# Optimization experiments

Hardware: AMD Instinct MI355X
Metric: run time of the kernel (lower is better)

## Reference

```python
import jax, jax.numpy as jnp
import numpy as np

B, T, I, H = 2048, 1024, 4, 16

def setup_inputs() -> dict:
    key = jax.random.key(0)
    ks = jax.random.split(key, 8)
    s_ih = 1.0 / np.sqrt(H)
    # PyTorch LSTM params: gate order [i, f, g, o], each block of size H
    W_ih = jax.random.uniform(ks[0], (4 * H, I), jnp.float32, -s_ih, s_ih)
    W_hh = jax.random.uniform(ks[1], (4 * H, H), jnp.float32, -s_ih, s_ih)
    b_ih = jax.random.uniform(ks[2], (4 * H,), jnp.float32, -s_ih, s_ih)
    b_hh = jax.random.uniform(ks[3], (4 * H,), jnp.float32, -s_ih, s_ih)
    W_d = jax.random.uniform(ks[4], (1, H), jnp.float32, -s_ih, s_ih)
    b_d = jax.random.uniform(ks[5], (1,), jnp.float32, -s_ih, s_ih)
    x = jax.random.normal(ks[6], (B, T, I), jnp.float32)
    return {"x": x, "W_ih": W_ih, "W_hh": W_hh, "b_ih": b_ih, "b_hh": b_hh, "W_d": W_d, "b_d": b_d}

def _lstm(x, W_ih, W_hh, b_ih, b_hh):
    # Precompute input projections for all timesteps: [B, T, 4H]
    xw = jnp.einsum('bti,gi->btg', x, W_ih) + b_ih + b_hh
    xw = jnp.swapaxes(xw, 0, 1)  # [T, B, 4H] for scan
    h0 = jnp.zeros((x.shape[0], W_hh.shape[1]), x.dtype)
    c0 = jnp.zeros_like(h0)
    Hh = W_hh.shape[1]

    def step(carry, xw_t):
        h, c = carry
        gates = xw_t + h @ W_hh.T  # [B, 4H]
        i = jax.nn.sigmoid(gates[:, 0*Hh:1*Hh])
        f = jax.nn.sigmoid(gates[:, 1*Hh:2*Hh])
        g = jnp.tanh(gates[:, 2*Hh:3*Hh])
        o = jax.nn.sigmoid(gates[:, 3*Hh:4*Hh])
        c = f * c + i * g
        h = o * jnp.tanh(c)
        return (h, c), h

    _, hs = jax.lax.scan(step, (h0, c0), xw)  # hs: [T, B, H]
    return jnp.swapaxes(hs, 0, 1)  # [B, T, H]

def reference(x, W_ih, W_hh, b_ih, b_hh, W_d, b_d):
    lstm_out = _lstm(x, W_ih, W_hh, b_ih, b_hh)
    return jax.nn.sigmoid(lstm_out @ W_d.T + b_d)  # [B, T, 1]
```

## Files before the change

kernel.cpp:

```cpp
#include <hip/hip_runtime.h>


#define T_DIM 1024
#define LOG2E 1.4426950408889634f

__device__ __forceinline__ float fsig(float x) {
    float e = __builtin_amdgcn_exp2f(-x * LOG2E);
    return __builtin_amdgcn_rcpf(1.0f + e);
}

template<int CTRL>
__device__ __forceinline__ float dpp_f(float v) {
    int i = __float_as_int(v);
    return __int_as_float(__builtin_amdgcn_update_dpp(i, i, CTRL, 0xF, 0xF, false));
}

__device__ __forceinline__ float swz16(float v) {
    return __int_as_float(__builtin_amdgcn_ds_swizzle(__float_as_int(v), 0x401F));
}

__global__ __launch_bounds__(64) void lstm_disc_kernel(
    const float* __restrict__ x,
    const float* __restrict__ W_ih,
    const float* __restrict__ W_hh,
    const float* __restrict__ b_ih,
    const float* __restrict__ b_hh,
    const float* __restrict__ W_d,
    const float* __restrict__ b_d,
    float* __restrict__ out)
{
    const int tid  = threadIdx.x;
    const int half = tid >> 5;
    const int s    = tid & 31;
    const int j    = s & 15;
    const int hi   = (s >> 4) & 1;
    const int batch = blockIdx.x * 2 + half;
    const int r1 = s, r2 = s + 32;

    float W1p[16], W2p[16], Wdp[16];
#pragma unroll
    for (int k = 0; k < 16; ++k) {
        const int jx = j ^ k;
        W1p[k] = W_hh[r1 * 16 + jx];
        W2p[k] = W_hh[r2 * 16 + jx];
        Wdp[k] = W_d[jx];
    }
    const float4 Wx1 = *reinterpret_cast<const float4*>(W_ih + r1 * 4);
    const float4 Wx2 = *reinterpret_cast<const float4*>(W_ih + r2 * 4);
    const float bias1 = b_ih[r1] + b_hh[r1];
    const float bias2 = b_ih[r2] + b_hh[r2];
    const float bd = b_d[0];
    const float m2  = hi ? 1.0f : 2.0f;
    const float m2c = m2 - 1.0f;

    const float4* xp = reinterpret_cast<const float4*>(x + (size_t)batch * (T_DIM * 4));
    float4 xv = xp[0];

    float h = 0.0f, c = 0.0f;
    float s0 = 0.f, s1 = 0.f, s2 = 0.f, s3 = 0.f;

    for (int t4 = 0; t4 < T_DIM; t4 += 4) {
#pragma unroll
        for (int u = 0; u < 4; ++u) {
            const int t = t4 + u;
            const float4 xn = xp[(t + 1 < T_DIM) ? (t + 1) : (T_DIM - 1)];

            float A0 = W1p[0] * h, B0 = W2p[0] * h, P0 = Wdp[0] * h;
            float A1 = 0.f, B1 = 0.f, P1 = 0.f;

            const float v1 = dpp_f<0xB1>(h);
            const float v2 = dpp_f<0x4E>(h);
            const float v3 = dpp_f<0x1B>(h);
            const float m7 = dpp_f<0x141>(h);
            const float mF = dpp_f<0x140>(h);
            A1 = fmaf(W1p[1], v1, A1); B1 = fmaf(W2p[1], v1, B1); P1 = fmaf(Wdp[1], v1, P1);
            A0 = fmaf(W1p[2], v2, A0); B0 = fmaf(W2p[2], v2, B0); P0 = fmaf(Wdp[2], v2, P0);
            A1 = fmaf(W1p[3], v3, A1); B1 = fmaf(W2p[3], v3, B1); P1 = fmaf(Wdp[3], v3, P1);
            const float v6 = dpp_f<0xB1>(m7);
            const float v5 = dpp_f<0x4E>(m7);
            const float v4 = dpp_f<0x1B>(m7);
            const float m8 = dpp_f<0x141>(mF);
            A0 = fmaf(W1p[7], m7, A0); B0 = fmaf(W2p[7], m7, B0); P0 = fmaf(Wdp[7], m7, P0);
            A1 = fmaf(W1p[6], v6, A1); B1 = fmaf(W2p[6], v6, B1); P1 = fmaf(Wdp[6], v6, P1);
            A0 = fmaf(W1p[5], v5, A0); B0 = fmaf(W2p[5], v5, B0); P0 = fmaf(Wdp[5], v5, P0);
            A1 = fmaf(W1p[4], v4, A1); B1 = fmaf(W2p[4], v4, B1); P1 = fmaf(Wdp[4], v4, P1);
            const float vE = dpp_f<0xB1>(mF);
            const float vD = dpp_f<0x4E>(mF);
            const float vC = dpp_f<0x1B>(mF);
            A0 = fmaf(W1p[15], mF, A0); B0 = fmaf(W2p[15], mF, B0); P0 = fmaf(Wdp[15], mF, P0);
            A1 = fmaf(W1p[14], vE, A1); B1 = fmaf(W2p[14], vE, B1); P1 = fmaf(Wdp[14], vE, P1);
            A0 = fmaf(W1p[13], vD, A0); B0 = fmaf(W2p[13], vD, B0); P0 = fmaf(Wdp[13], vD, P0);
            A1 = fmaf(W1p[12], vC, A1); B1 = fmaf(W2p[12], vC, B1); P1 = fmaf(Wdp[12], vC, P1);
            const float v9 = dpp_f<0xB1>(m8);
            const float vA = dpp_f<0x4E>(m8);
            const float vB = dpp_f<0x1B>(m8);
            A0 = fmaf(W1p[8],  m8, A0); B0 = fmaf(W2p[8],  m8, B0); P0 = fmaf(Wdp[8],  m8, P0);
            A1 = fmaf(W1p[9],  v9, A1); B1 = fmaf(W2p[9],  v9, B1); P1 = fmaf(Wdp[9],  v9, P1);
            A0 = fmaf(W1p[10], vA, A0); B0 = fmaf(W2p[10], vA, B0); P0 = fmaf(Wdp[10], vA, P0);
            A1 = fmaf(W1p[11], vB, A1); B1 = fmaf(W2p[11], vB, B1); P1 = fmaf(Wdp[11], vB, P1);

            float g1 = fmaf(Wx1.x, xv.x, fmaf(Wx1.y, xv.y, fmaf(Wx1.z, xv.z, fmaf(Wx1.w, xv.w, bias1))));
            float g2 = fmaf(Wx2.x, xv.x, fmaf(Wx2.y, xv.y, fmaf(Wx2.z, xv.z, fmaf(Wx2.w, xv.w, bias2))));
            g1 += A0 + A1;
            g2 += B0 + B1;

            const float oo = fsig((P0 + P1) + bd);
            if (u == 1) s0 = oo;
            else if (u == 2) s1 = oo;
            else if (u == 3) s2 = oo;
            else {
                s3 = oo;
                if (t4 > 0 && (tid & 31) == 0)
                    *reinterpret_cast<float4*>(out + (size_t)batch * T_DIM + (t4 - 4)) =
                        make_float4(s0, s1, s2, s3);
            }

            const float act1 = fsig(g1);
            const float act2 = fmaf(m2, fsig(m2 * g2), -m2c);
            const float sw1 = swz16(act1);
            const float sw2 = swz16(act2);
            const float ig = hi ? (sw1 * sw2) : (act1 * act2);
            const float f  = hi ? act1 : sw1;
            const float o  = hi ? act2 : sw2;
            c = fmaf(f, c, ig);
            const float tc = fmaf(2.0f, fsig(2.0f * c), -1.0f);
            h = o * tc;

            xv = xn;
        }
    }

    {
        float P0 = Wdp[0] * h, P1 = 0.f;
        const float v1 = dpp_f<0xB1>(h);
        const float v2 = dpp_f<0x4E>(h);
        const float v3 = dpp_f<0x1B>(h);
        const float m7 = dpp_f<0x141>(h);
        const float mF = dpp_f<0x140>(h);
        P1 = fmaf(Wdp[1], v1, P1); P0 = fmaf(Wdp[2], v2, P0); P1 = fmaf(Wdp[3], v3, P1);
        const float v6 = dpp_f<0xB1>(m7);
        const float v5 = dpp_f<0x4E>(m7);
        const float v4 = dpp_f<0x1B>(m7);
        const float m8 = dpp_f<0x141>(mF);
        P0 = fmaf(Wdp[7], m7, P0); P1 = fmaf(Wdp[6], v6, P1);
        P0 = fmaf(Wdp[5], v5, P0); P1 = fmaf(Wdp[4], v4, P1);
        const float vE = dpp_f<0xB1>(mF);
        const float vD = dpp_f<0x4E>(mF);
        const float vC = dpp_f<0x1B>(mF);
        P0 = fmaf(Wdp[15], mF, P0); P1 = fmaf(Wdp[14], vE, P1);
        P0 = fmaf(Wdp[13], vD, P0); P1 = fmaf(Wdp[12], vC, P1);
        const float v9 = dpp_f<0xB1>(m8);
        const float vA = dpp_f<0x4E>(m8);
        const float vB = dpp_f<0x1B>(m8);
        P0 = fmaf(Wdp[8],  m8, P0); P1 = fmaf(Wdp[9],  v9, P1);
        P0 = fmaf(Wdp[10], vA, P0); P1 = fmaf(Wdp[11], vB, P1);

        s3 = fsig((P0 + P1) + bd);
        if ((tid & 31) == 0)
            *reinterpret_cast<float4*>(out + (size_t)batch * T_DIM + (T_DIM - 4)) =
                make_float4(s0, s1, s2, s3);
    }
}

extern "C" void kernel_launch(void* const* d_in, const int* in_sizes, int n_in,
                              void* d_out, int out_size, void* d_ws, size_t ws_size,
                              hipStream_t stream) {
    const float* x    = (const float*)d_in[0];
    const float* W_ih = (const float*)d_in[1];
    const float* W_hh = (const float*)d_in[2];
    const float* b_ih = (const float*)d_in[3];
    const float* b_hh = (const float*)d_in[4];
    const float* W_d  = (const float*)d_in[5];
    const float* b_d  = (const float*)d_in[6];
    float* out = (float*)d_out;

    lstm_disc_kernel<<<1024, 64, 0, stream>>>(x, W_ih, W_hh, b_ih, b_hh, W_d, b_d, out);
}
```

Baseline: 339.9 us.

## Map one batch per wave with one gate row per lane

```diff
diff --git a/kernel.cpp b/kernel.cpp
--- a/kernel.cpp
+++ b/kernel.cpp
@@ -3,6 +3,8 @@
 
 #define T_DIM 1024
 #define LOG2E 1.4426950408889634f
+
+typedef __attribute__((ext_vector_type(2))) int i32x2;
 
 __device__ __forceinline__ float fsig(float x) {
     float e = __builtin_amdgcn_exp2f(-x * LOG2E);
@@ -19,6 +21,16 @@
     return __int_as_float(__builtin_amdgcn_ds_swizzle(__float_as_int(v), 0x401F));
 }
 
+__device__ __forceinline__ float xchg32(float v, bool hi32) {
+#if __has_builtin(__builtin_amdgcn_permlane32_swap)
+    i32x2 pr = __builtin_amdgcn_permlane32_swap(__float_as_int(v), __float_as_int(v), false, false);
+    return __int_as_float(hi32 ? pr[0] : pr[1]);
+#else
+    int l = threadIdx.x & 63;
+    return __int_as_float(__builtin_amdgcn_ds_bpermute(((l ^ 32) << 2), __float_as_int(v)));
+#endif
+}
+
 __global__ __launch_bounds__(64) void lstm_disc_kernel(
     const float* __restrict__ x,
     const float* __restrict__ W_ih,
@@ -29,35 +41,28 @@
     const float* __restrict__ b_d,
     float* __restrict__ out)
 {
-    const int tid  = threadIdx.x;
-    const int half = tid >> 5;
-    const int s    = tid & 31;
-    const int j    = s & 15;
-    const int hi   = (s >> 4) & 1;
-    const int batch = blockIdx.x * 2 + half;
-    const int r1 = s, r2 = s + 32;
+    const int l  = threadIdx.x;
+    const int j  = l & 15;
+    const bool s1 = (l & 16) != 0;
+    const bool s2 = (l & 32) != 0;
+    const int batch = blockIdx.x;
 
-    float W1p[16], W2p[16], Wdp[16];
+    float Wp[16];
 #pragma unroll
-    for (int k = 0; k < 16; ++k) {
-        const int jx = j ^ k;
-        W1p[k] = W_hh[r1 * 16 + jx];
-        W2p[k] = W_hh[r2 * 16 + jx];
-        Wdp[k] = W_d[jx];
-    }
-    const float4 Wx1 = *reinterpret_cast<const float4*>(W_ih + r1 * 4);
-    const float4 Wx2 = *reinterpret_cast<const float4*>(W_ih + r2 * 4);
-    const float bias1 = b_ih[r1] + b_hh[r1];
-    const float bias2 = b_ih[r2] + b_hh[r2];
+    for (int k = 0; k < 16; ++k) Wp[k] = W_hh[l * 16 + (j ^ k)];
+    const float4 Wx = *reinterpret_cast<const float4*>(W_ih + l * 4);
+    const float bias = b_ih[l] + b_hh[l];
+    const float wd = W_d[j];
     const float bd = b_d[0];
-    const float m2  = hi ? 1.0f : 2.0f;
-    const float m2c = m2 - 1.0f;
+    const bool isg = s2 && !s1;
+    const float m2  = isg ? 2.0f : 1.0f;
+    const float m2n = isg ? -1.0f : 0.0f;
 
     const float4* xp = reinterpret_cast<const float4*>(x + (size_t)batch * (T_DIM * 4));
     float4 xv = xp[0];
 
     float h = 0.0f, c = 0.0f;
-    float s0 = 0.f, s1 = 0.f, s2 = 0.f, s3 = 0.f;
+    float s0v = 0.f, s1v = 0.f, s2v = 0.f;
 
     for (int t4 = 0; t4 < T_DIM; t4 += 4) {
 #pragma unroll
@@ -65,100 +70,77 @@
             const int t = t4 + u;
             const float4 xn = xp[(t + 1 < T_DIM) ? (t + 1) : (T_DIM - 1)];
 
-            float A0 = W1p[0] * h, B0 = W2p[0] * h, P0 = Wdp[0] * h;
-            float A1 = 0.f, B1 = 0.f, P1 = 0.f;
+            const float gx = fmaf(Wx.x, xv.x, fmaf(Wx.y, xv.y,
+                               fmaf(Wx.z, xv.z, fmaf(Wx.w, xv.w, bias))));
 
+            float a0 = fmaf(Wp[0], h, gx);
             const float v1 = dpp_f<0xB1>(h);
             const float v2 = dpp_f<0x4E>(h);
             const float v3 = dpp_f<0x1B>(h);
             const float m7 = dpp_f<0x141>(h);
             const float mF = dpp_f<0x140>(h);
-            A1 = fmaf(W1p[1], v1, A1); B1 = fmaf(W2p[1], v1, B1); P1 = fmaf(Wdp[1], v1, P1);
-            A0 = fmaf(W1p[2], v2, A0); B0 = fmaf(W2p[2], v2, B0); P0 = fmaf(Wdp[2], v2, P0);
-            A1 = fmaf(W1p[3], v3, A1); B1 = fmaf(W2p[3], v3, B1); P1 = fmaf(Wdp[3], v3, P1);
+            float a1 = Wp[1] * v1;
+            float a2 = Wp[2] * v2;
+            float a3 = Wp[3] * v3;
             const float v6 = dpp_f<0xB1>(m7);
             const float v5 = dpp_f<0x4E>(m7);
             const float v4 = dpp_f<0x1B>(m7);
             const float m8 = dpp_f<0x141>(mF);
-            A0 = fmaf(W1p[7], m7, A0); B0 = fmaf(W2p[7], m7, B0); P0 = fmaf(Wdp[7], m7, P0);
-            A1 = fmaf(W1p[6], v6, A1); B1 = fmaf(W2p[6], v6, B1); P1 = fmaf(Wdp[6], v6, P1);
-            A0 = fmaf(W1p[5], v5, A0); B0 = fmaf(W2p[5], v5, B0); P0 = fmaf(Wdp[5], v5, P0);
-            A1 = fmaf(W1p[4], v4, A1); B1 = fmaf(W2p[4], v4, B1); P1 = fmaf(Wdp[4], v4, P1);
+            a0 = fmaf(Wp[7], m7, a0);
+            a1 = fmaf(Wp[6], v6, a1);
+            a2 = fmaf(Wp[5], v5, a2);
+            a3 = fmaf(Wp[4], v4, a3);
             const float vE = dpp_f<0xB1>(mF);
             const float vD = dpp_f<0x4E>(mF);
             const float vC = dpp_f<0x1B>(mF);
-            A0 = fmaf(W1p[15], mF, A0); B0 = fmaf(W2p[15], mF, B0); P0 = fmaf(Wdp[15], mF, P0);
-            A1 = fmaf(W1p[14], vE, A1); B1 = fmaf(W2p[14], vE, B1); P1 = fmaf(Wdp[14], vE, P1);
-            A0 = fmaf(W1p[13], vD, A0); B0 = fmaf(W2p[13], vD, B0); P0 = fmaf(Wdp[13], vD, P0);
-            A1 = fmaf(W1p[12], vC, A1); B1 = fmaf(W2p[12], vC, B1); P1 = fmaf(Wdp[12], vC, P1);
+            a0 = fmaf(Wp[15], mF, a0);
+            a1 = fmaf(Wp[14], vE, a1);
+            a2 = fmaf(Wp[13], vD, a2);
+            a3 = fmaf(Wp[12], vC, a3);
             const float v9 = dpp_f<0xB1>(m8);
             const float vA = dpp_f<0x4E>(m8);
             const float vB = dpp_f<0x1B>(m8);
-            A0 = fmaf(W1p[8],  m8, A0); B0 = fmaf(W2p[8],  m8, B0); P0 = fmaf(Wdp[8],  m8, P0);
-            A1 = fmaf(W1p[9],  v9, A1); B1 = fmaf(W2p[9],  v9, B1); P1 = fmaf(Wdp[9],  v9, P1);
-            A0 = fmaf(W1p[10], vA, A0); B0 = fmaf(W2p[10], vA, B0); P0 = fmaf(Wdp[10], vA, P0);
-            A1 = fmaf(W1p[11], vB, A1); B1 = fmaf(W2p[11], vB, B1); P1 = fmaf(Wdp[11], vB, P1);
+            a0 = fmaf(Wp[8],  m8, a0);
+            a1 = fmaf(Wp[9],  v9, a1);
+            a2 = fmaf(Wp[10], vA, a2);
+            a3 = fmaf(Wp[11], vB, a3);
+            const float g = (a0 + a1) + (a2 + a3);
 
-            float g1 = fmaf(Wx1.x, xv.x, fmaf(Wx1.y, xv.y, fmaf(Wx1.z, xv.z, fmaf(Wx1.w, xv.w, bias1))));
-            float g2 = fmaf(Wx2.x, xv.x, fmaf(Wx2.y, xv.y, fmaf(Wx2.z, xv.z, fmaf(Wx2.w, xv.w, bias2))));
-            g1 += A0 + A1;
-            g2 += B0 + B1;
+            const float act = fmaf(m2, fsig(m2 * g), m2n);
 
-            const float oo = fsig((P0 + P1) + bd);
-            if (u == 1) s0 = oo;
-            else if (u == 2) s1 = oo;
-            else if (u == 3) s2 = oo;
-            else {
-                s3 = oo;
-                if (t4 > 0 && (tid & 31) == 0)
-                    *reinterpret_cast<float4*>(out + (size_t)batch * T_DIM + (t4 - 4)) =
-                        make_float4(s0, s1, s2, s3);
-            }
+            const float b16 = swz16(act);
+            const float b32 = xchg32(act, s2);
+            const float b48 = swz16(b32);
+            const float pa = s1 ? b16 : act;
+            const float pb = s1 ? b48 : b32;
+            const float ig = pa * pb;
+            const float f1 = s2 ? b48 : b16;
+            const float f2 = s2 ? b32 : act;
+            const float fg = s1 ? f2 : f1;
+            const float o1 = s2 ? b16 : b48;
+            const float o2 = s2 ? act : b32;
+            const float og = s1 ? o2 : o1;
 
-            const float act1 = fsig(g1);
-            const float act2 = fmaf(m2, fsig(m2 * g2), -m2c);
-            const float sw1 = swz16(act1);
-            const float sw2 = swz16(act2);
-            const float ig = hi ? (sw1 * sw2) : (act1 * act2);
-            const float f  = hi ? act1 : sw1;
-            const float o  = hi ? act2 : sw2;
-            c = fmaf(f, c, ig);
+            c = fmaf(fg, c, ig);
             const float tc = fmaf(2.0f, fsig(2.0f * c), -1.0f);
-            h = o * tc;
+            h = og * tc;
+
+            float p = h * wd;
+            p += dpp_f<0xB1>(p);
+            p += dpp_f<0x4E>(p);
+            p += dpp_f<0x124>(p);
+            p += dpp_f<0x128>(p);
+            const float oo = fsig(p + bd);
+
+            if (u == 0) s0v = oo;
+            else if (u == 1) s1v = oo;
+            else if (u == 2) s2v = oo;
+            else if (l == 0)
+                *reinterpret_cast<float4*>(out + (size_t)batch * T_DIM + t4) =
+                    make_float4(s0v, s1v, s2v, oo);
 
             xv = xn;
         }
-    }
-
-    {
-        float P0 = Wdp[0] * h, P1 = 0.f;
-        const float v1 = dpp_f<0xB1>(h);
-        const float v2 = dpp_f<0x4E>(h);
-        const float v3 = dpp_f<0x1B>(h);
-        const float m7 = dpp_f<0x141>(h);
-        const float mF = dpp_f<0x140>(h);
-        P1 = fmaf(Wdp[1], v1, P1); P0 = fmaf(Wdp[2], v2, P0); P1 = fmaf(Wdp[3], v3, P1);
-        const float v6 = dpp_f<0xB1>(m7);
-        const float v5 = dpp_f<0x4E>(m7);
-        const float v4 = dpp_f<0x1B>(m7);
-        const float m8 = dpp_f<0x141>(mF);
-        P0 = fmaf(Wdp[7], m7, P0); P1 = fmaf(Wdp[6], v6, P1);
-        P0 = fmaf(Wdp[5], v5, P0); P1 = fmaf(Wdp[4], v4, P1);
-        const float vE = dpp_f<0xB1>(mF);
-        const float vD = dpp_f<0x4E>(mF);
-        const float vC = dpp_f<0x1B>(mF);
-        P0 = fmaf(Wdp[15], mF, P0); P1 = fmaf(Wdp[14], vE, P1);
-        P0 = fmaf(Wdp[13], vD, P0); P1 = fmaf(Wdp[12], vC, P1);
-        const float v9 = dpp_f<0xB1>(m8);
-        const float vA = dpp_f<0x4E>(m8);
-        const float vB = dpp_f<0x1B>(m8);
-        P0 = fmaf(Wdp[8],  m8, P0); P1 = fmaf(Wdp[9],  v9, P1);
-        P0 = fmaf(Wdp[10], vA, P0); P1 = fmaf(Wdp[11], vB, P1);
-
-        s3 = fsig((P0 + P1) + bd);
-        if ((tid & 31) == 0)
-            *reinterpret_cast<float4*>(out + (size_t)batch * T_DIM + (T_DIM - 4)) =
-                make_float4(s0, s1, s2, s3);
     }
 }
 
@@ -174,5 +156,5 @@
     const float* b_d  = (const float*)d_in[6];
     float* out = (float*)d_out;
 
-    lstm_disc_kernel<<<1024, 64, 0, stream>>>(x, W_ih, W_hh, b_ih, b_hh, W_d, b_d, out);
+    lstm_disc_kernel<<<2048, 64, 0, stream>>>(x, W_ih, W_hh, b_ih, b_hh, W_d, b_d, out);
 }
```

Measured after the change: 482.3 us. +41.9%, slower.
